# Kernel tuning notes

Measured on AMD Instinct MI355X. Metric: run time of the kernel, lower is better.

Reference implementation:

```python
import jax, jax.numpy as jnp
import numpy as np

NEG_SLOPE = 0.2
B, N, F_IN = 8, 256, 64
HID, EDGE_F = 128, 64


def setup_inputs() -> dict:
    key = jax.random.key(0)
    ks = jax.random.split(key, 8)
    src = jax.random.normal(ks[0], (B, N, F_IN), dtype=jnp.float32)
    adj = jax.random.randint(ks[1], (B, N, N), 0, 2, dtype=jnp.int32)
    mask = jnp.ones((B, N, N), dtype=jnp.int32)
    # params (xavier-ish scaling)
    W_lin = jax.random.normal(ks[2], (HID, F_IN), dtype=jnp.float32) * (1.0 / np.sqrt(F_IN))
    a_src = jax.random.normal(ks[3], (HID, 1), dtype=jnp.float32) * (1.414 / np.sqrt(HID))
    a_dst = jax.random.normal(ks[4], (HID, 1), dtype=jnp.float32) * (1.414 / np.sqrt(HID))
    W_edge = jax.random.normal(ks[5], (EDGE_F, 1), dtype=jnp.float32) * 1.414
    a_edge = jax.random.normal(ks[6], (EDGE_F, 1), dtype=jnp.float32) * (1.414 / np.sqrt(EDGE_F))
    return {"src": src, "adj": adj, "mask": mask, "W_lin": W_lin,
            "a_src": a_src, "a_dst": a_dst, "W_edge": W_edge, "a_edge": a_edge}


def _pairwise_norm(src):
    # ||src_i - src_j||_2 over feature dim, safe at the zero diagonal
    d = src[:, :, None, :] - src[:, None, :, :]          # [B,N,N,F]
    sq = jnp.sum(d * d, axis=-1)                          # [B,N,N]
    safe = jnp.where(sq > 0, sq, 1.0)
    return jnp.where(sq > 0, jnp.sqrt(safe), 0.0)


def reference(src, adj, mask, W_lin, a_src, a_dst, W_edge, a_edge):
    x = jnp.einsum('bnf,hf->bnh', src, W_lin)             # lin (no bias)
    x = jax.nn.leaky_relu(x, NEG_SLOPE)
    attn_s = x @ a_src                                    # [B,N,1]
    attn_d = x @ a_dst                                    # [B,N,1]
    e = attn_s + jnp.swapaxes(attn_d, 1, 2)               # [B,N,N]
    # lin_edge(d[...,None]) @ a_edge == d * (W_edge . a_edge), a scalar coef
    coef = jnp.dot(W_edge[:, 0], a_edge[:, 0])
    edge = _pairwise_norm(src) * coef                     # [B,N,N]
    e = e + edge * adj.astype(e.dtype)
    a = e * mask.astype(e.dtype)
    return jax.nn.softmax(a, axis=-1)
```

## Files before the change

### kernel.cpp

```cpp
#include <hip/hip_runtime.h>
#include <math.h>

#define BB 8
#define NN 256
#define F_IN 64
#define HID 128
constexpr float NEG_SLOPE = 0.2f;

__global__ void __launch_bounds__(128) attn_sd_kernel(
    const float* __restrict__ src, const float* __restrict__ W_lin,
    const float* __restrict__ a_src, const float* __restrict__ a_dst,
    const float* __restrict__ W_edge, const float* __restrict__ a_edge,
    float* __restrict__ sd)
{
    const int blk = blockIdx.x;
    const int t = threadIdx.x;
    const int BN = BB * NN;

    if (blk == BN) {
        float v = (t < 64) ? W_edge[t] * a_edge[t] : 0.0f;
        #pragma unroll
        for (int off = 32; off > 0; off >>= 1) v += __shfl_down(v, off);
        if (t == 0) sd[2 * BN] = v;
        return;
    }

    __shared__ float s_src[F_IN];
    if (t < F_IN) s_src[t] = src[blk * F_IN + t];
    __syncthreads();

    const float4* w4 = reinterpret_cast<const float4*>(W_lin + t * F_IN);
    float acc = 0.0f;
    #pragma unroll
    for (int f4 = 0; f4 < F_IN / 4; ++f4) {
        float4 w = w4[f4];
        acc += w.x * s_src[f4 * 4 + 0] + w.y * s_src[f4 * 4 + 1]
             + w.z * s_src[f4 * 4 + 2] + w.w * s_src[f4 * 4 + 3];
    }
    float x = acc > 0.0f ? acc : NEG_SLOPE * acc;
    float sv = x * a_src[t];
    float dv = x * a_dst[t];

    #pragma unroll
    for (int off = 32; off > 0; off >>= 1) {
        sv += __shfl_down(sv, off);
        dv += __shfl_down(dv, off);
    }
    __shared__ float red[4];
    const int wave = t >> 6, lane = t & 63;
    if (lane == 0) { red[wave * 2 + 0] = sv; red[wave * 2 + 1] = dv; }
    __syncthreads();
    if (t == 0) {
        sd[blk]      = red[0] + red[2];
        sd[BN + blk] = red[1] + red[3];
    }
}

__global__ void __launch_bounds__(256) attn_row_kernel(
    const float* __restrict__ src, const int* __restrict__ adj,
    const int* __restrict__ mask, const float* __restrict__ sd,
    float* __restrict__ out)
{
    const int blk = blockIdx.x;
    const int b = blk >> 8;
    const int j = threadIdx.x;
    const int BN = BB * NN;

    __shared__ float s_i[F_IN];
    if (j < F_IN) s_i[j] = src[blk * F_IN + j];
    __syncthreads();

    const float coef = sd[2 * BN];
    const float si   = sd[blk];
    const float dj   = sd[BN + b * NN + j];

    const float4* sj4 = reinterpret_cast<const float4*>(src + (b * NN + j) * F_IN);
    float sq = 0.0f;
    #pragma unroll
    for (int f4 = 0; f4 < F_IN / 4; ++f4) {
        float4 v = sj4[f4];
        float d0 = s_i[f4 * 4 + 0] - v.x;
        float d1 = s_i[f4 * 4 + 1] - v.y;
        float d2 = s_i[f4 * 4 + 2] - v.z;
        float d3 = s_i[f4 * 4 + 3] - v.w;
        sq += d0 * d0 + d1 * d1 + d2 * d2 + d3 * d3;
    }
    const float nrm = sq > 0.0f ? sqrtf(sq) : 0.0f;

    const float e = si + dj + nrm * coef * (float)adj[blk * NN + j];
    const float a = e * (float)mask[blk * NN + j];

    __shared__ float red[4];
    __shared__ float bcast;

    float m = a;
    #pragma unroll
    for (int off = 32; off > 0; off >>= 1) m = fmaxf(m, __shfl_down(m, off));
    const int wave = j >> 6, lane = j & 63;
    if (lane == 0) red[wave] = m;
    __syncthreads();
    if (j == 0) bcast = fmaxf(fmaxf(red[0], red[1]), fmaxf(red[2], red[3]));
    __syncthreads();
    const float rowmax = bcast;

    const float ex = expf(a - rowmax);
    float ssum = ex;
    #pragma unroll
    for (int off = 32; off > 0; off >>= 1) ssum += __shfl_down(ssum, off);
    __syncthreads();
    if (lane == 0) red[wave] = ssum;
    __syncthreads();
    if (j == 0) bcast = 1.0f / (red[0] + red[1] + red[2] + red[3]);
    __syncthreads();

    out[blk * NN + j] = ex * bcast;
}

extern "C" void kernel_launch(void* const* d_in, const int* in_sizes, int n_in,
                              void* d_out, int out_size, void* d_ws, size_t ws_size,
                              hipStream_t stream) {
    const float* src    = (const float*)d_in[0];
    const int*   adj    = (const int*)  d_in[1];
    const int*   mask   = (const int*)  d_in[2];
    const float* W_lin  = (const float*)d_in[3];
    const float* a_src  = (const float*)d_in[4];
    const float* a_dst  = (const float*)d_in[5];
    const float* W_edge = (const float*)d_in[6];
    const float* a_edge = (const float*)d_in[7];
    float* out = (float*)d_out;
    float* sd  = (float*)d_ws;

    attn_sd_kernel<<<BB * NN + 1, 128, 0, stream>>>(src, W_lin, a_src, a_dst,
                                                    W_edge, a_edge, sd);
    attn_row_kernel<<<BB * NN, 256, 0, stream>>>(src, adj, mask, sd, out);
}
```

Before: 95.66 us.

## Stage transposed weights and batch features in LDS, process multiple rows per block

The projection kernel now stages W_lin transposed in shared memory and handles two nodes per block. The row kernel loads the whole batch's src features transposed into LDS once, keeps column j's features in registers, and loops over four rows per block. The aim is to cut repeated global loads of src and W_lin and spread block setup over more work. The cost is the full-matrix staging per block (about 66KB of LDS in the row kernel), 64 registers per thread for pj, fewer blocks, and serialized per-row reductions with barriers.

```diff
diff --git a/kernel.cpp b/kernel.cpp
--- a/kernel.cpp
+++ b/kernel.cpp
@@ -6,8 +6,9 @@
 #define F_IN 64
 #define HID 128
 constexpr float NEG_SLOPE = 0.2f;
+#define BN (BB * NN)
 
-__global__ void __launch_bounds__(128) attn_sd_kernel(
+__global__ void __launch_bounds__(256) attn_sd_kernel(
     const float* __restrict__ src, const float* __restrict__ W_lin,
     const float* __restrict__ a_src, const float* __restrict__ a_dst,
     const float* __restrict__ W_edge, const float* __restrict__ a_edge,
@@ -15,44 +16,60 @@
 {
     const int blk = blockIdx.x;
     const int t = threadIdx.x;
-    const int BN = BB * NN;
 
-    if (blk == BN) {
+    if (blk == BN / 2) {
         float v = (t < 64) ? W_edge[t] * a_edge[t] : 0.0f;
-        #pragma unroll
-        for (int off = 32; off > 0; off >>= 1) v += __shfl_down(v, off);
-        if (t == 0) sd[2 * BN] = v;
+        if (t < 64) {
+            #pragma unroll
+            for (int off = 32; off > 0; off >>= 1) v += __shfl_down(v, off);
+            if (t == 0) sd[2 * BN] = v;
+        }
         return;
     }
 
-    __shared__ float s_src[F_IN];
-    if (t < F_IN) s_src[t] = src[blk * F_IN + t];
+    __shared__ float WT[F_IN * 129];
+    __shared__ float s_src[2][F_IN];
+    __shared__ float red[4][2];
+
+    #pragma unroll
+    for (int k = 0; k < 8; ++k) {
+        int idx4 = t + k * 256;
+        int h = idx4 >> 4;
+        int f4 = idx4 & 15;
+        float4 w = reinterpret_cast<const float4*>(W_lin)[idx4];
+        WT[(4 * f4 + 0) * 129 + h] = w.x;
+        WT[(4 * f4 + 1) * 129 + h] = w.y;
+        WT[(4 * f4 + 2) * 129 + h] = w.z;
+        WT[(4 * f4 + 3) * 129 + h] = w.w;
+    }
+    if (t < 2 * F_IN) s_src[t >> 6][t & 63] = src[blk * (2 * F_IN) + t];
     __syncthreads();
 
-    const float4* w4 = reinterpret_cast<const float4*>(W_lin + t * F_IN);
+    const int half = t >> 7;
+    const int h = t & 127;
     float acc = 0.0f;
     #pragma unroll
-    for (int f4 = 0; f4 < F_IN / 4; ++f4) {
-        float4 w = w4[f4];
-        acc += w.x * s_src[f4 * 4 + 0] + w.y * s_src[f4 * 4 + 1]
-             + w.z * s_src[f4 * 4 + 2] + w.w * s_src[f4 * 4 + 3];
-    }
+    for (int f = 0; f < F_IN; ++f)
+        acc = fmaf(WT[f * 129 + h], s_src[half][f], acc);
     float x = acc > 0.0f ? acc : NEG_SLOPE * acc;
-    float sv = x * a_src[t];
-    float dv = x * a_dst[t];
+    float sv = x * a_src[h];
+    float dv = x * a_dst[h];
 
     #pragma unroll
     for (int off = 32; off > 0; off >>= 1) {
         sv += __shfl_down(sv, off);
         dv += __shfl_down(dv, off);
     }
-    __shared__ float red[4];
     const int wave = t >> 6, lane = t & 63;
-    if (lane == 0) { red[wave * 2 + 0] = sv; red[wave * 2 + 1] = dv; }
+    if (lane == 0) { red[wave][0] = sv; red[wave][1] = dv; }
     __syncthreads();
     if (t == 0) {
-        sd[blk]      = red[0] + red[2];
-        sd[BN + blk] = red[1] + red[3];
+        sd[2 * blk]      = red[0][0] + red[1][0];
+        sd[BN + 2 * blk] = red[0][1] + red[1][1];
+    }
+    if (t == 128) {
+        sd[2 * blk + 1]      = red[2][0] + red[3][0];
+        sd[BN + 2 * blk + 1] = red[2][1] + red[3][1];
     }
 }
 
@@ -62,58 +79,70 @@
     float* __restrict__ out)
 {
     const int blk = blockIdx.x;
-    const int b = blk >> 8;
     const int j = threadIdx.x;
-    const int BN = BB * NN;
+    const int b = blk >> 6;
 
-    __shared__ float s_i[F_IN];
-    if (j < F_IN) s_i[j] = src[blk * F_IN + j];
+    __shared__ float pT[F_IN * 257];
+    __shared__ float redm[4], reds[4];
+    __shared__ float bc[2];
+
+    const float* srcb = src + b * NN * F_IN;
+    #pragma unroll
+    for (int k = 0; k < 16; ++k) {
+        int idx4 = j + k * 256;
+        int n = idx4 >> 4;
+        int f4 = idx4 & 15;
+        float4 v = reinterpret_cast<const float4*>(srcb)[idx4];
+        pT[(4 * f4 + 0) * 257 + n] = v.x;
+        pT[(4 * f4 + 1) * 257 + n] = v.y;
+        pT[(4 * f4 + 2) * 257 + n] = v.z;
+        pT[(4 * f4 + 3) * 257 + n] = v.w;
+    }
     __syncthreads();
 
+    float pj[F_IN];
+    #pragma unroll
+    for (int f = 0; f < F_IN; ++f) pj[f] = pT[f * 257 + j];
+
+    const float dj   = sd[BN + b * NN + j];
     const float coef = sd[2 * BN];
-    const float si   = sd[blk];
-    const float dj   = sd[BN + b * NN + j];
+    const int wave = j >> 6, lane = j & 63;
 
-    const float4* sj4 = reinterpret_cast<const float4*>(src + (b * NN + j) * F_IN);
-    float sq = 0.0f;
-    #pragma unroll
-    for (int f4 = 0; f4 < F_IN / 4; ++f4) {
-        float4 v = sj4[f4];
-        float d0 = s_i[f4 * 4 + 0] - v.x;
-        float d1 = s_i[f4 * 4 + 1] - v.y;
-        float d2 = s_i[f4 * 4 + 2] - v.z;
-        float d3 = s_i[f4 * 4 + 3] - v.w;
-        sq += d0 * d0 + d1 * d1 + d2 * d2 + d3 * d3;
+    for (int r = 0; r < 4; ++r) {
+        const int grow = blk * 4 + r;
+        const int il = grow & (NN - 1);
+        const float si = sd[grow];
+
+        float sq = 0.0f;
+        #pragma unroll
+        for (int f = 0; f < F_IN; ++f) {
+            float d = pT[f * 257 + il] - pj[f];
+            sq = fmaf(d, d, sq);
+        }
+        const float nrm = sq > 0.0f ? sqrtf(sq) : 0.0f;
+
+        const float e = si + dj + nrm * coef * (float)adj[grow * NN + j];
+        const float a = e * (float)mask[grow * NN + j];
+
+        float m = a;
+        #pragma unroll
+        for (int off = 32; off > 0; off >>= 1) m = fmaxf(m, __shfl_down(m, off));
+        if (lane == 0) redm[wave] = m;
+        __syncthreads();
+        if (j == 0) bc[0] = fmaxf(fmaxf(redm[0], redm[1]), fmaxf(redm[2], redm[3]));
+        __syncthreads();
+        const float ex = expf(a - bc[0]);
+
+        float ssum = ex;
+        #pragma unroll
+        for (int off = 32; off > 0; off >>= 1) ssum += __shfl_down(ssum, off);
+        if (lane == 0) reds[wave] = ssum;
+        __syncthreads();
+        if (j == 0) bc[1] = 1.0f / (reds[0] + reds[1] + reds[2] + reds[3]);
+        __syncthreads();
+
+        out[grow * NN + j] = ex * bc[1];
     }
-    const float nrm = sq > 0.0f ? sqrtf(sq) : 0.0f;
-
-    const float e = si + dj + nrm * coef * (float)adj[blk * NN + j];
-    const float a = e * (float)mask[blk * NN + j];
-
-    __shared__ float red[4];
-    __shared__ float bcast;
-
-    float m = a;
-    #pragma unroll
-    for (int off = 32; off > 0; off >>= 1) m = fmaxf(m, __shfl_down(m, off));
-    const int wave = j >> 6, lane = j & 63;
-    if (lane == 0) red[wave] = m;
-    __syncthreads();
-    if (j == 0) bcast = fmaxf(fmaxf(red[0], red[1]), fmaxf(red[2], red[3]));
-    __syncthreads();
-    const float rowmax = bcast;
-
-    const float ex = expf(a - rowmax);
-    float ssum = ex;
-    #pragma unroll
-    for (int off = 32; off > 0; off >>= 1) ssum += __shfl_down(ssum, off);
-    __syncthreads();
-    if (lane == 0) red[wave] = ssum;
-    __syncthreads();
-    if (j == 0) bcast = 1.0f / (red[0] + red[1] + red[2] + red[3]);
-    __syncthreads();
-
-    out[blk * NN + j] = ex * bcast;
 }
 
 extern "C" void kernel_launch(void* const* d_in, const int* in_sizes, int n_in,
@@ -130,7 +159,7 @@
     float* out = (float*)d_out;
     float* sd  = (float*)d_ws;
 
-    attn_sd_kernel<<<BB * NN + 1, 128, 0, stream>>>(src, W_lin, a_src, a_dst,
-                                                    W_edge, a_edge, sd);
-    attn_row_kernel<<<BB * NN, 256, 0, stream>>>(src, adj, mask, sd, out);
+    attn_sd_kernel<<<BN / 2 + 1, 256, 0, stream>>>(src, W_lin, a_src, a_dst,
+                                                   W_edge, a_edge, sd);
+    attn_row_kernel<<<BN / 4, 256, 0, stream>>>(src, adj, mask, sd, out);
 }
```

New measurement: 82.34 us. -13.9%, faster.
